# Optimization experiments

Measured on AMD Instinct MI355X. Metric: run time of the kernel, lower is better.

The kernel has to match this reference:

```python
import jax, jax.numpy as jnp
import numpy as np

E = 256  # embedding_dim
H = 256  # hidden_dim
B = 65536


def setup_inputs() -> dict:
    key = jax.random.key(0)
    ks = jax.random.split(key, 15)
    inp = {
        "x": jax.random.normal(ks[0], (B, E), dtype=jnp.float32),
        "c": jax.random.normal(ks[1], (B, H), dtype=jnp.float32),
        "h": jax.random.normal(ks[2], (B, H), dtype=jnp.float32),
    }
    names = ["W_i", "U_i", "b_i", "W_f", "U_f", "b_f", "W_c", "U_c", "b_c", "W_o", "U_o", "b_o"]
    shapes = [(E, H), (H, H), (H,)] * 4
    for n, s, k in zip(names, shapes, ks[3:]):
        inp[n] = jax.random.normal(k, s, dtype=jnp.float32)
    return inp


def reference(x, c, h, W_i, U_i, b_i, W_f, U_f, b_f, W_c, U_c, b_c, W_o, U_o, b_o):
    # Batch the four input/hidden projections into two GEMMs, then fuse gates.
    W = jnp.concatenate([W_f, W_i, W_o, W_c], axis=1)  # [E, 4H]
    U = jnp.concatenate([U_f, U_i, U_o, U_c], axis=1)  # [H, 4H]
    b = jnp.concatenate([b_f, b_i, b_o, b_c], axis=0)  # [4H]
    z = x @ W + h @ U + b                               # [B, 4H]
    zf, zi, zo, zg = jnp.split(z, 4, axis=1)
    f = jax.nn.sigmoid(zf)
    i = jax.nn.sigmoid(zi)
    o = jax.nn.sigmoid(zo)
    g = jnp.tanh(zg)
    c_new = c * f + g * i
    h_new = o * jnp.tanh(c_new)
    return (c_new, h_new)
```

## Files before the change

kernel.cpp:

```cpp
#include <hip/hip_runtime.h>
#include <hip/hip_fp16.h>

typedef _Float16 half8 __attribute__((ext_vector_type(8)));
typedef float f32x4 __attribute__((ext_vector_type(4)));

#define BHSZ 16777216

__device__ __forceinline__ void gload16(const void* g, const void* lds) {
  __builtin_amdgcn_global_load_lds((const __attribute__((address_space(1))) void*)g,
                                   (__attribute__((address_space(3))) void*)lds,
                                   16, 0, 0);
}

__device__ __forceinline__ float fast_sigmoid(float z) {
  float e = __builtin_amdgcn_exp2f(-z * 1.4426950408889634f);
  return __builtin_amdgcn_rcpf(1.0f + e);
}

__device__ __forceinline__ float fast_tanh(float z) {
  float a = __builtin_fabsf(z);
  float e = __builtin_amdgcn_exp2f(a * 2.8853900817779268f);
  float t = 1.0f - 2.0f * __builtin_amdgcn_rcpf(1.0f + e);
  return z < 0.0f ? -t : t;
}

__global__ __launch_bounds__(256) void pack_a(const float* __restrict__ x,
                                              const float* __restrict__ h,
                                              _Float16* __restrict__ Apk) {
  long i = (long)blockIdx.x * 256 + threadIdx.x;
  long e = i * 8;
  int b = (int)(e >> 9);
  int k = (int)(e & 511);
  const float* src = (k < 256) ? (x + (long)b * 256 + k)
                               : (h + (long)b * 256 + (k - 256));
  float4 v0 = reinterpret_cast<const float4*>(src)[0];
  float4 v1 = reinterpret_cast<const float4*>(src)[1];
  half8 o;
  o[0] = (_Float16)v0.x; o[1] = (_Float16)v0.y;
  o[2] = (_Float16)v0.z; o[3] = (_Float16)v0.w;
  o[4] = (_Float16)v1.x; o[5] = (_Float16)v1.y;
  o[6] = (_Float16)v1.z; o[7] = (_Float16)v1.w;
  *reinterpret_cast<half8*>(Apk + e) = o;
}

__global__ __launch_bounds__(256) void pack_b(
    const float* __restrict__ Wf, const float* __restrict__ Uf,
    const float* __restrict__ Wi, const float* __restrict__ Ui,
    const float* __restrict__ Wo, const float* __restrict__ Uo,
    const float* __restrict__ Wc, const float* __restrict__ Uc,
    _Float16* __restrict__ Bp) {
  int idx = blockIdx.x * 256 + threadIdx.x;
  int k = idx & 511;
  int Np = idx >> 9;
  int g = (Np >> 4) & 3;
  int cl = ((Np >> 6) << 4) | (Np & 15);
  const float* W;
  const float* U;
  switch (g) {
    case 0: W = Wf; U = Uf; break;
    case 1: W = Wi; U = Ui; break;
    case 2: W = Wo; U = Uo; break;
    default: W = Wc; U = Uc; break;
  }
  float v = (k < 256) ? W[k * 256 + cl] : U[(k - 256) * 256 + cl];
  Bp[idx] = (_Float16)v;
}

__global__ __launch_bounds__(512, 2) void lstm_gemm(
    const _Float16* __restrict__ Apk, const _Float16* __restrict__ Bp,
    const float* __restrict__ cin,
    const float* __restrict__ bf_, const float* __restrict__ bi_,
    const float* __restrict__ bo_, const float* __restrict__ bc_,
    float* __restrict__ out) {
  __shared__ __align__(16) char smem[131072];

  int tid = threadIdx.x;
  int w = tid >> 6, l = tid & 63;
  int l15 = l & 15, lg = l >> 4;
  int wr = w >> 2, wcn = w & 3;

  int bid = blockIdx.x;
  int wg = (bid & 7) * 128 + (bid >> 3);
  int bm = wg >> 2, bn = wg & 3;

  int rpl = tid >> 3, s8 = tid & 7;
  int i8 = s8 ^ (rpl & 7);
  int rbase = 2 * rpl + (i8 >> 2);
  int csrc = (i8 & 3) * 8;
  long sA = ((long)bm * 256 + rbase) * 512 + csrc;
  long sB = ((long)bn * 256 + rbase) * 512 + csrc;
  int wb1k = w * 1024;

  int offA[8], offB[4];
#pragma unroll
  for (int mf = 0; mf < 8; ++mf) {
    int r = wr * 128 + mf * 16 + l15;
    int rp = r >> 1;
    offA[mf] = rp * 128 + (((((r & 1) << 2) | lg) ^ (rp & 7)) << 4);
  }
#pragma unroll
  for (int nf = 0; nf < 4; ++nf) {
    int r = wcn * 64 + nf * 16 + l15;
    int rp = r >> 1;
    offB[nf] = 32768 + rp * 128 + (((((r & 1) << 2) | lg) ^ (rp & 7)) << 4);
  }

  f32x4 acc[8][4];
#pragma unroll
  for (int a2 = 0; a2 < 8; ++a2)
#pragma unroll
    for (int b2 = 0; b2 < 4; ++b2)
      acc[a2][b2] = (f32x4){0.f, 0.f, 0.f, 0.f};

  auto stageA = [&](int ktn, int hf, char* dbuf) {
    const _Float16* s0 = Apk + sA + (long)ktn * 64 + (long)hf * 128 * 512;
    gload16(s0, dbuf + hf * 8192 + wb1k);
    gload16(s0 + 32, dbuf + 16384 + hf * 8192 + wb1k);
  };
  auto stageB = [&](int ktn, int hf, char* dbuf) {
    const _Float16* s0 = Bp + sB + (long)ktn * 64 + (long)hf * 128 * 512;
    gload16(s0, dbuf + 32768 + hf * 8192 + wb1k);
    gload16(s0 + 32, dbuf + 49152 + hf * 8192 + wb1k);
  };

  stageA(0, 0, smem);
  stageA(0, 1, smem);
  stageB(0, 0, smem);
  stageB(0, 1, smem);

#pragma unroll
  for (int kt = 0; kt < 8; ++kt) {
    __syncthreads();
    const char* rb = smem + (kt & 1) * 65536;
    char* wbuf = smem + ((kt + 1) & 1) * 65536;
    half8 av[4], bv[4];

    if (kt < 7) stageA(kt + 1, 0, wbuf);
#pragma unroll
    for (int nf = 0; nf < 4; ++nf)
      bv[nf] = *reinterpret_cast<const half8*>(rb + offB[nf]);
#pragma unroll
    for (int q = 0; q < 4; ++q)
      av[q] = *reinterpret_cast<const half8*>(rb + offA[q]);
    __builtin_amdgcn_s_setprio(1);
#pragma unroll
    for (int q = 0; q < 4; ++q)
#pragma unroll
      for (int nf = 0; nf < 4; ++nf)
        acc[q][nf] = __builtin_amdgcn_mfma_f32_16x16x32_f16(
            av[q], bv[nf], acc[q][nf], 0, 0, 0);
    __builtin_amdgcn_s_setprio(0);

    if (kt < 7) stageA(kt + 1, 1, wbuf);
#pragma unroll
    for (int q = 0; q < 4; ++q)
      av[q] = *reinterpret_cast<const half8*>(rb + offA[4 + q]);
    __builtin_amdgcn_s_setprio(1);
#pragma unroll
    for (int q = 0; q < 4; ++q)
#pragma unroll
      for (int nf = 0; nf < 4; ++nf)
        acc[4 + q][nf] = __builtin_amdgcn_mfma_f32_16x16x32_f16(
            av[q], bv[nf], acc[4 + q][nf], 0, 0, 0);
    __builtin_amdgcn_s_setprio(0);

    if (kt < 7) stageB(kt + 1, 0, wbuf);
#pragma unroll
    for (int nf = 0; nf < 4; ++nf)
      bv[nf] = *reinterpret_cast<const half8*>(rb + 16384 + offB[nf]);
#pragma unroll
    for (int q = 0; q < 4; ++q)
      av[q] = *reinterpret_cast<const half8*>(rb + 16384 + offA[q]);
    __builtin_amdgcn_s_setprio(1);
#pragma unroll
    for (int q = 0; q < 4; ++q)
#pragma unroll
      for (int nf = 0; nf < 4; ++nf)
        acc[q][nf] = __builtin_amdgcn_mfma_f32_16x16x32_f16(
            av[q], bv[nf], acc[q][nf], 0, 0, 0);
    __builtin_amdgcn_s_setprio(0);

    if (kt < 7) stageB(kt + 1, 1, wbuf);
#pragma unroll
    for (int q = 0; q < 4; ++q)
      av[q] = *reinterpret_cast<const half8*>(rb + 16384 + offA[4 + q]);
    __builtin_amdgcn_s_setprio(1);
#pragma unroll
    for (int q = 0; q < 4; ++q)
#pragma unroll
      for (int nf = 0; nf < 4; ++nf)
        acc[4 + q][nf] = __builtin_amdgcn_mfma_f32_16x16x32_f16(
            av[q], bv[nf], acc[4 + q][nf], 0, 0, 0);
    __builtin_amdgcn_s_setprio(0);
  }

  int col = (bn * 4 + wcn) * 16 + l15;
  float vbf = bf_[col], vbi = bi_[col], vbo = bo_[col], vbc = bc_[col];
#pragma unroll
  for (int mf = 0; mf < 8; ++mf) {
#pragma unroll
    for (int r = 0; r < 4; ++r) {
      long row = (long)(bm * 256 + wr * 128 + mf * 16 + lg * 4 + r);
      float zf = acc[mf][0][r] + vbf;
      float zi = acc[mf][1][r] + vbi;
      float zo = acc[mf][2][r] + vbo;
      float zg = acc[mf][3][r] + vbc;
      float fg = fast_sigmoid(zf);
      float ig = fast_sigmoid(zi);
      float og = fast_sigmoid(zo);
      float gg = fast_tanh(zg);
      float cv = cin[row * 256 + col];
      float cn = cv * fg + gg * ig;
      float hn = og * fast_tanh(cn);
      out[row * 256 + col] = cn;
      out[BHSZ + row * 256 + col] = hn;
    }
  }
}

extern "C" void kernel_launch(void* const* d_in, const int* in_sizes, int n_in,
                              void* d_out, int out_size, void* d_ws, size_t ws_size,
                              hipStream_t stream) {
  const float* x  = (const float*)d_in[0];
  const float* c  = (const float*)d_in[1];
  const float* h  = (const float*)d_in[2];
  const float* Wi = (const float*)d_in[3];
  const float* Ui = (const float*)d_in[4];
  const float* bi = (const float*)d_in[5];
  const float* Wf = (const float*)d_in[6];
  const float* Uf = (const float*)d_in[7];
  const float* bf = (const float*)d_in[8];
  const float* Wc = (const float*)d_in[9];
  const float* Uc = (const float*)d_in[10];
  const float* bc = (const float*)d_in[11];
  const float* Wo = (const float*)d_in[12];
  const float* Uo = (const float*)d_in[13];
  const float* bo = (const float*)d_in[14];

  _Float16* Apk = (_Float16*)d_ws;
  _Float16* Bp  = (_Float16*)((char*)d_ws + (size_t)65536 * 512 * 2);

  pack_a<<<16384, 256, 0, stream>>>(x, h, Apk);
  pack_b<<<2048, 256, 0, stream>>>(Wf, Uf, Wi, Ui, Wo, Uo, Wc, Uc, Bp);
  lstm_gemm<<<1024, 512, 0, stream>>>(Apk, Bp, c, bf, bi, bo, bc,
                                      (float*)d_out);
}
```

Before: 143.2 us.

## Replace double-buffered K loop with four-stage LDS ring using vmcnt waits

Restructures the GEMM main loop from 8 double-buffered 64-wide K tiles into 16 smaller 32-wide K tiles held in a 4-slot LDS ring with three stages in flight. Manual s_waitcnt vmcnt counters plus a raw s_barrier replace __syncthreads, so global loads stay outstanding longer and overlap with MFMA work. This adds deeper prefetch at the cost of twice as many barriers and relies on exact vmcnt accounting, which risks a race if the compiler emits other vector memory ops.

```diff
diff --git a/kernel.cpp b/kernel.cpp
--- a/kernel.cpp
+++ b/kernel.cpp
@@ -5,6 +5,7 @@
 typedef float f32x4 __attribute__((ext_vector_type(4)));
 
 #define BHSZ 16777216
+#define SBAR() __builtin_amdgcn_s_barrier()
 
 __device__ __forceinline__ void gload16(const void* g, const void* lds) {
   __builtin_amdgcn_global_load_lds((const __attribute__((address_space(1))) void*)g,
@@ -102,7 +103,7 @@
   for (int nf = 0; nf < 4; ++nf) {
     int r = wcn * 64 + nf * 16 + l15;
     int rp = r >> 1;
-    offB[nf] = 32768 + rp * 128 + (((((r & 1) << 2) | lg) ^ (rp & 7)) << 4);
+    offB[nf] = 16384 + rp * 128 + (((((r & 1) << 2) | lg) ^ (rp & 7)) << 4);
   }
 
   f32x4 acc[8][4];
@@ -112,85 +113,48 @@
     for (int b2 = 0; b2 < 4; ++b2)
       acc[a2][b2] = (f32x4){0.f, 0.f, 0.f, 0.f};
 
-  auto stageA = [&](int ktn, int hf, char* dbuf) {
-    const _Float16* s0 = Apk + sA + (long)ktn * 64 + (long)hf * 128 * 512;
-    gload16(s0, dbuf + hf * 8192 + wb1k);
-    gload16(s0 + 32, dbuf + 16384 + hf * 8192 + wb1k);
+  auto stage = [&](int js) {
+    char* db = smem + (js & 3) * 32768;
+    long ko = (long)js * 32;
+#pragma unroll
+    for (int hf = 0; hf < 2; ++hf)
+      gload16(Apk + sA + ko + (long)hf * 128 * 512, db + hf * 8192 + wb1k);
+#pragma unroll
+    for (int hf = 0; hf < 2; ++hf)
+      gload16(Bp + sB + ko + (long)hf * 128 * 512,
+              db + 16384 + hf * 8192 + wb1k);
   };
-  auto stageB = [&](int ktn, int hf, char* dbuf) {
-    const _Float16* s0 = Bp + sB + (long)ktn * 64 + (long)hf * 128 * 512;
-    gload16(s0, dbuf + 32768 + hf * 8192 + wb1k);
-    gload16(s0 + 32, dbuf + 49152 + hf * 8192 + wb1k);
-  };
-
-  stageA(0, 0, smem);
-  stageA(0, 1, smem);
-  stageB(0, 0, smem);
-  stageB(0, 1, smem);
-
-#pragma unroll
-  for (int kt = 0; kt < 8; ++kt) {
-    __syncthreads();
-    const char* rb = smem + (kt & 1) * 65536;
-    char* wbuf = smem + ((kt + 1) & 1) * 65536;
-    half8 av[4], bv[4];
-
-    if (kt < 7) stageA(kt + 1, 0, wbuf);
+
+  stage(0);
+  stage(1);
+  stage(2);
+
+#pragma unroll
+  for (int j = 0; j < 16; ++j) {
+    if (j <= 13)
+      asm volatile("s_waitcnt vmcnt(8)" ::: "memory");
+    else if (j == 14)
+      asm volatile("s_waitcnt vmcnt(4)" ::: "memory");
+    else
+      asm volatile("s_waitcnt vmcnt(0)" ::: "memory");
+    SBAR();
+    if (j <= 12) stage(j + 3);
+
+    const char* sb = smem + (j & 3) * 32768;
+    half8 bv[4], av[8];
 #pragma unroll
     for (int nf = 0; nf < 4; ++nf)
-      bv[nf] = *reinterpret_cast<const half8*>(rb + offB[nf]);
-#pragma unroll
-    for (int q = 0; q < 4; ++q)
-      av[q] = *reinterpret_cast<const half8*>(rb + offA[q]);
+      bv[nf] = *reinterpret_cast<const half8*>(sb + offB[nf]);
+#pragma unroll
+    for (int mf = 0; mf < 8; ++mf)
+      av[mf] = *reinterpret_cast<const half8*>(sb + offA[mf]);
     __builtin_amdgcn_s_setprio(1);
 #pragma unroll
-    for (int q = 0; q < 4; ++q)
+    for (int mf = 0; mf < 8; ++mf)
 #pragma unroll
       for (int nf = 0; nf < 4; ++nf)
-        acc[q][nf] = __builtin_amdgcn_mfma_f32_16x16x32_f16(
-            av[q], bv[nf], acc[q][nf], 0, 0, 0);
-    __builtin_amdgcn_s_setprio(0);
-
-    if (kt < 7) stageA(kt + 1, 1, wbuf);
-#pragma unroll
-    for (int q = 0; q < 4; ++q)
-      av[q] = *reinterpret_cast<const half8*>(rb + offA[4 + q]);
-    __builtin_amdgcn_s_setprio(1);
-#pragma unroll
-    for (int q = 0; q < 4; ++q)
-#pragma unroll
-      for (int nf = 0; nf < 4; ++nf)
-        acc[4 + q][nf] = __builtin_amdgcn_mfma_f32_16x16x32_f16(
-            av[q], bv[nf], acc[4 + q][nf], 0, 0, 0);
-    __builtin_amdgcn_s_setprio(0);
-
-    if (kt < 7) stageB(kt + 1, 0, wbuf);
-#pragma unroll
-    for (int nf = 0; nf < 4; ++nf)
-      bv[nf] = *reinterpret_cast<const half8*>(rb + 16384 + offB[nf]);
-#pragma unroll
-    for (int q = 0; q < 4; ++q)
-      av[q] = *reinterpret_cast<const half8*>(rb + 16384 + offA[q]);
-    __builtin_amdgcn_s_setprio(1);
-#pragma unroll
-    for (int q = 0; q < 4; ++q)
-#pragma unroll
-      for (int nf = 0; nf < 4; ++nf)
-        acc[q][nf] = __builtin_amdgcn_mfma_f32_16x16x32_f16(
-            av[q], bv[nf], acc[q][nf], 0, 0, 0);
-    __builtin_amdgcn_s_setprio(0);
-
-    if (kt < 7) stageB(kt + 1, 1, wbuf);
-#pragma unroll
-    for (int q = 0; q < 4; ++q)
-      av[q] = *reinterpret_cast<const half8*>(rb + 16384 + offA[4 + q]);
-    __builtin_amdgcn_s_setprio(1);
-#pragma unroll
-    for (int q = 0; q < 4; ++q)
-#pragma unroll
-      for (int nf = 0; nf < 4; ++nf)
-        acc[4 + q][nf] = __builtin_amdgcn_mfma_f32_16x16x32_f16(
-            av[q], bv[nf], acc[4 + q][nf], 0, 0, 0);
+        acc[mf][nf] = __builtin_amdgcn_mfma_f32_16x16x32_f16(
+            av[mf], bv[nf], acc[mf][nf], 0, 0, 0);
     __builtin_amdgcn_s_setprio(0);
   }
 
```

Result: slower. 148.6 us (+3.7%).
